# Kernel tuning notes

Measured on AMD Instinct MI355X. Metric: run time of the kernel, lower is better.

## Reference

```python
import jax, jax.numpy as jnp
import numpy as np

P = 1048576   # total sampled points
N = 8192      # rays
E = 8         # experts
H = 128       # expert hidden dim
TOP_K = 2
INTERVAL = 0.5      # stepsize * voxel_size_ratio
ACT_SHIFT = -4.0    # models[-1].act_shift
THRESH = 1e-4       # fast_color_thres (ndc=False)


def raw2alpha(d):
    # Raw2Alpha: alpha = 1 - exp(-softplus(density + act_shift) * interval)
    return 1.0 - jnp.exp(-jax.nn.softplus(d + ACT_SHIFT) * INTERVAL)


def alphas2weights(alpha, ray_id, n_rays):
    # Sequential per-ray transmittance: w_j = alpha_j * prod_{k<j in ray}(1 - alpha_k)
    la = jnp.log1p(-jnp.clip(alpha, 0.0, 1.0 - 1e-6))      # [P], <= 0
    cum = jnp.cumsum(la)
    excl = cum - la                                          # exclusive cumsum, nonincreasing
    # offset per ray = excl at first point of the (sorted) segment == segment max
    offset = jax.ops.segment_max(excl, ray_id, num_segments=n_rays)
    T = jnp.exp(excl - offset[ray_id])                       # transmittance before each point
    weights = alpha * T
    alphainv_last = jnp.exp(jax.ops.segment_sum(la, ray_id, num_segments=n_rays))
    return weights, alphainv_last


def setup_inputs() -> dict:
    key = jax.random.key(0)
    ks = jax.random.split(key, 12)
    s = 0.3  # weight scale keeping activations in a sane range
    return {
        "ray_pts": jax.random.uniform(ks[0], (P, 3), dtype=jnp.float32),
        "viewdirs": jax.random.normal(ks[1], (N, 3), dtype=jnp.float32),
        "bg": jnp.ones((3,), dtype=jnp.float32),
        "Wd1": jax.random.normal(ks[2], (3, H), dtype=jnp.float32) * s,
        "bd1": jnp.zeros((H,), dtype=jnp.float32),
        "Wd2": jax.random.normal(ks[3], (H, 1), dtype=jnp.float32) * s,
        "Wg": jax.random.normal(ks[4], (6, E), dtype=jnp.float32) * s,
        "We1": jax.random.normal(ks[5], (E, 6, H), dtype=jnp.float32) * s,
        "be1": jnp.zeros((E, H), dtype=jnp.float32),
        "Wrgb": jax.random.normal(ks[6], (E, H, 3), dtype=jnp.float32) * s,
        "Walpha": jax.random.normal(ks[7], (E, H, 1), dtype=jnp.float32) * s,
        "ray_id": jnp.sort(jax.random.randint(ks[8], (P,), 0, N)).astype(jnp.int32),
    }


def reference(ray_pts, viewdirs, bg, Wd1, bd1, Wd2, Wg, We1, be1, Wrgb, Walpha, ray_id):
    # --- density grid query + activation ---
    hd = jax.nn.relu(ray_pts @ Wd1 + bd1)                    # [P,H]
    density = (hd @ Wd2)[:, 0]                               # [P]
    alpha0 = raw2alpha(density)
    # filter low density (zeroing alpha == dropping the point from the cumprod)
    alpha0 = jnp.where(alpha0 > THRESH, alpha0, 0.0)
    w0, _ = alphas2weights(alpha0, ray_id, N)
    # filter low transmittance (w0 <= THRESH also covers alpha0 == 0)
    keep = w0 > THRESH                                        # [P] bool

    # --- gate: softmax over experts, top-k, renormalize ---
    x = jnp.concatenate([ray_pts, viewdirs[ray_id]], axis=-1)  # [P,6]
    probs = jax.nn.softmax(x @ Wg, axis=-1)                    # [P,E]
    vals, idx = jax.lax.top_k(probs, TOP_K)                    # [P,K]
    vals = vals / jnp.sum(vals, axis=-1, keepdims=True)        # top_k > 1
    g = jnp.sum(vals[..., None] * jax.nn.one_hot(idx, E, dtype=vals.dtype), axis=1)  # [P,E]
    g = g * keep[:, None].astype(g.dtype)

    # --- per-expert radiance / alpha, mixed by gate weights ---
    rgb = jnp.zeros((ray_pts.shape[0], 3), dtype=ray_pts.dtype)
    alpha_mix = jnp.zeros((ray_pts.shape[0],), dtype=ray_pts.dtype)
    for e in range(E):  # fixed small expert count
        h = jax.nn.relu(x @ We1[e] + be1[e])                   # [P,H]
        rgb_e = jax.nn.sigmoid(h @ Wrgb[e])                    # [P,3]
        a_e = raw2alpha((h @ Walpha[e])[:, 0])                 # [P]
        rgb = rgb + g[:, e:e + 1] * rgb_e
        alpha_mix = alpha_mix + g[:, e] * a_e

    # --- composite: Alphas2Weights + segment_coo sum + background ---
    w, alphainv_last = alphas2weights(alpha_mix, ray_id, N)
    rgb_marched = jax.ops.segment_sum(w[:, None] * rgb, ray_id, num_segments=N)
    rgb_marched = rgb_marched + alphainv_last[:, None] * bg
    return rgb_marched
```

## Files before the change

kernel.cpp:

```cpp
#include <hip/hip_runtime.h>

#define PTOT   1048576
#define NRAYS  8192
#define THRESH 1e-4f
#define ECAP   PTOT

typedef float F2 __attribute__((ext_vector_type(2)));

__device__ __forceinline__ F2 f2splat(float s){ F2 r; r.x = s; r.y = s; return r; }
__device__ __forceinline__ F2 f2fma(F2 a, float b, F2 c){
    return __builtin_elementwise_fma(a, f2splat(b), c);
}
__device__ __forceinline__ float raw2alpha_f(float d){
    return 1.0f - rsqrtf(1.0f + __expf(d - 4.0f));
}

__global__ __launch_bounds__(256) void k_point(
    const float* __restrict__ pts, const float* __restrict__ vdirs,
    const int* __restrict__ ray_id,
    const float* __restrict__ Wd1, const float* __restrict__ bd1,
    const float* __restrict__ Wd2, const float* __restrict__ Wg,
    float* __restrict__ alpha0, float* __restrict__ g0a, int* __restrict__ eea,
    int* __restrict__ ray_off)
{
    __shared__ float4 WD4[128];
    __shared__ float  WD2s[128];
    __shared__ float  WGs[8][6];
    int t = threadIdx.x;
    if (t < 128){
        WD4[t] = make_float4(Wd1[t], Wd1[128+t], Wd1[256+t], bd1[t]);
        WD2s[t] = Wd2[t];
    }
    if (t < 48) WGs[t & 7][t >> 3] = Wg[t];
    __syncthreads();

    int base = blockIdx.x * 1024 + t;
    F2 px[2], py[2], pz[2], vx[2], vy[2], vz[2], dens[2];
    int rid0[2], rid1[2];
    #pragma unroll
    for (int q=0;q<2;q++){
        int p0 = base + (2*q)*256, p1 = p0 + 256;
        px[q] = (F2){pts[3*p0],   pts[3*p1]};
        py[q] = (F2){pts[3*p0+1], pts[3*p1+1]};
        pz[q] = (F2){pts[3*p0+2], pts[3*p1+2]};
        int r0 = ray_id[p0], r1 = ray_id[p1];
        rid0[q] = r0; rid1[q] = r1;
        vx[q] = (F2){vdirs[3*r0],   vdirs[3*r1]};
        vy[q] = (F2){vdirs[3*r0+1], vdirs[3*r1+1]};
        vz[q] = (F2){vdirs[3*r0+2], vdirs[3*r1+2]};
        dens[q] = f2splat(0.f);
    }
    #pragma unroll
    for (int q=0;q<2;q++){
        int p0 = base + (2*q)*256, p1 = p0 + 256;
        int prev0 = (p0 == 0) ? -1 : ray_id[p0-1];
        if (prev0 != rid0[q]) for (int r=prev0+1; r<=rid0[q]; ++r) ray_off[r] = p0;
        int prev1 = ray_id[p1-1];
        if (prev1 != rid1[q]) for (int r=prev1+1; r<=rid1[q]; ++r) ray_off[r] = p1;
        if (p1 == PTOT-1) for (int r=rid1[q]+1; r<=NRAYS; ++r) ray_off[r] = PTOT;
    }
    #pragma unroll 2
    for (int i=0;i<128;i++){
        float4 w = WD4[i]; float w2 = WD2s[i];
        #pragma unroll
        for (int q=0;q<2;q++){
            F2 h = f2fma(px[q], w.x, f2fma(py[q], w.y, f2fma(pz[q], w.z, f2splat(w.w))));
            h = __builtin_elementwise_max(h, f2splat(0.f));
            dens[q] = f2fma(h, w2, dens[q]);
        }
    }
    #pragma unroll
    for (int q=0;q<2;q++){
        float a0 = raw2alpha_f(dens[q].x);
        float a1 = raw2alpha_f(dens[q].y);
        alpha0[base + (2*q)*256]   = (a0 > THRESH) ? a0 : 0.f;
        alpha0[base + (2*q+1)*256] = (a1 > THRESH) ? a1 : 0.f;
    }
    float m0[4], m1[4]; int i0[4], i1[4];
    #pragma unroll
    for (int j=0;j<4;j++){ m0[j]=-3.0e38f; m1[j]=-3.0e38f; i0[j]=0; i1[j]=0; }
    for (int e=0;e<8;e++){
        float w0=WGs[e][0],w1=WGs[e][1],w2=WGs[e][2],w3=WGs[e][3],w4=WGs[e][4],w5=WGs[e][5];
        #pragma unroll
        for (int q=0;q<2;q++){
            F2 l = f2fma(px[q],w0, f2fma(py[q],w1, f2fma(pz[q],w2,
                   f2fma(vx[q],w3, f2fma(vy[q],w4,
                   __builtin_elementwise_fma(vz[q], f2splat(w5), f2splat(0.f)))))));
            int j0 = 2*q, j1 = 2*q+1;
            float lx = l.x, ly = l.y;
            if (lx > m0[j0]){ m1[j0]=m0[j0]; i1[j0]=i0[j0]; m0[j0]=lx; i0[j0]=e; }
            else if (lx > m1[j0]){ m1[j0]=lx; i1[j0]=e; }
            if (ly > m0[j1]){ m1[j1]=m0[j1]; i1[j1]=i0[j1]; m0[j1]=ly; i0[j1]=e; }
            else if (ly > m1[j1]){ m1[j1]=ly; i1[j1]=e; }
        }
    }
    #pragma unroll
    for (int j=0;j<4;j++){
        float g0 = __fdividef(1.0f, 1.0f + __expf(m1[j]-m0[j]));
        g0a[base + j*256] = g0;
        eea[base + j*256] = i0[j] | (i1[j] << 8);
    }
}

__global__ __launch_bounds__(256) void k_scanfill(
    const float* __restrict__ alpha0, const int* __restrict__ eea,
    const float* __restrict__ g0a, const int* __restrict__ ray_off,
    unsigned char* __restrict__ keep, int* __restrict__ cntA,
    int2* __restrict__ ent)
{
    __shared__ int wcs[4][8];
    __shared__ int wb[4][8];
    int t = threadIdx.x, lane = t & 63, w = t >> 6;
    unsigned long long lt = (1ull << lane) - 1ull;
    int wid = blockIdx.x*4 + w;
    int s = ray_off[wid], e = ray_off[wid+1];

    int c[8];
    #pragma unroll
    for (int x=0;x<8;x++) c[x]=0;
    float carry = 1.f;
    for (int ch = s; ch < e; ch += 64){
        int p = ch + lane;
        bool in = p < e;
        float a = in ? alpha0[p] : 0.f;
        int  ee = in ? eea[p] : 0;
        float incl = 1.f - a;
        #pragma unroll
        for (int d=1; d<64; d<<=1){ float tt = __shfl_up(incl, d); if (lane >= d) incl *= tt; }
        float excl = __shfl_up(incl, 1); if (lane == 0) excl = 1.f;
        float w0 = a * carry * excl;
        int k = (in && w0 > THRESH) ? 1 : 0;
        if (in) keep[p] = (unsigned char)k;
        int e0 = ee & 255, e1 = (ee >> 8) & 255;
        #pragma unroll
        for (int x=0;x<8;x++){
            unsigned long long m0 = __ballot(k && e0==x);
            unsigned long long m1 = __ballot(k && e1==x);
            c[x] += __popcll(m0) + __popcll(m1);
        }
        carry *= __shfl(incl, 63);
    }
    if (lane == 0){
        #pragma unroll
        for (int x=0;x<8;x++) wcs[w][x] = c[x];
    }
    __syncthreads();
    if (t < 8){
        int tot = wcs[0][t]+wcs[1][t]+wcs[2][t]+wcs[3][t];
        int b = tot ? atomicAdd(&cntA[t], tot) : 0;
        wb[0][t] = b; b += wcs[0][t];
        wb[1][t] = b; b += wcs[1][t];
        wb[2][t] = b; b += wcs[2][t];
        wb[3][t] = b;
    }
    __syncthreads();
    int cur[8];
    #pragma unroll
    for (int x=0;x<8;x++) cur[x] = x*ECAP + wb[w][x];

    for (int ch = s; ch < e; ch += 64){
        int p = ch + lane;
        bool in = p < e;
        int  k  = in ? keep[p] : 0;
        int  ee = in ? eea[p] : 0;
        float g0 = in ? g0a[p] : 0.f;
        int e0 = ee & 255, e1 = (ee >> 8) & 255;
        #pragma unroll
        for (int x=0;x<8;x++){
            unsigned long long m0 = __ballot(k && e0==x);
            unsigned long long m1 = __ballot(k && e1==x);
            if (k && e0==x)
                ent[cur[x] + __popcll(m0 & lt)] = make_int2(p, __float_as_int(g0));
            if (k && e1==x)
                ent[cur[x] + __popcll(m0) + __popcll(m1 & lt)] =
                    make_int2(p | (1 << 30), __float_as_int(1.0f - g0));
            cur[x] += __popcll(m0) + __popcll(m1);
        }
    }
}

__global__ __launch_bounds__(256) void k_expert(
    const int2* __restrict__ ent, const int* __restrict__ cntA,
    const float* __restrict__ pts, const int* __restrict__ ray_id,
    const float* __restrict__ vdirs,
    const float* __restrict__ We1, const float* __restrict__ be1,
    const float* __restrict__ Wrgb, const float* __restrict__ Walpha,
    float4* __restrict__ res)
{
    int k = blockIdx.x;
    int e = -1, n = 0, base = 0;
    int acc = 0;
    #pragma unroll
    for (int i=0;i<8;i++){
        int c  = cntA[i];
        int ch = (c + 2047) >> 11;
        if (e < 0 && k < acc + ch){ e = i; n = c; base = (k - acc) << 11; }
        acc += ch;
    }
    if (e < 0) return;

    __shared__ float4 WA[128];
    __shared__ float4 WB[128];
    __shared__ float4 WC[128];
    int t = threadIdx.x;
    if (t < 128){
        const float* w = We1 + e*768;
        WA[t] = make_float4(w[t], w[128+t], w[256+t], w[384+t]);
        WB[t] = make_float4(w[512+t], w[640+t], be1[e*128+t], Walpha[e*128+t]);
        const float* wr = Wrgb + e*384 + 3*t;
        WC[t] = make_float4(wr[0], wr[1], wr[2], 0.f);
    }
    __syncthreads();
    const int2* eb = ent + (size_t)e * ECAP;

    F2 x0[4],x1[4],x2[4],x3[4],x4[4],x5[4];
    F2 ar[4],ag[4],ab[4],aa[4];
    #pragma unroll
    for (int pr=0;pr<4;pr++){
        int idx0 = base + t + (2*pr)*256, idx1 = idx0 + 256;
        int2 r0 = (idx0 < n) ? eb[idx0] : make_int2(0,0);
        int2 r1 = (idx1 < n) ? eb[idx1] : make_int2(0,0);
        int p0 = r0.x & 0x0FFFFFFF, p1 = r1.x & 0x0FFFFFFF;
        int ra = ray_id[p0], rb = ray_id[p1];
        x0[pr] = (F2){pts[3*p0],   pts[3*p1]};
        x1[pr] = (F2){pts[3*p0+1], pts[3*p1+1]};
        x2[pr] = (F2){pts[3*p0+2], pts[3*p1+2]};
        x3[pr] = (F2){vdirs[3*ra],   vdirs[3*rb]};
        x4[pr] = (F2){vdirs[3*ra+1], vdirs[3*rb+1]};
        x5[pr] = (F2){vdirs[3*ra+2], vdirs[3*rb+2]};
        ar[pr] = f2splat(0.f); ag[pr] = f2splat(0.f);
        ab[pr] = f2splat(0.f); aa[pr] = f2splat(0.f);
    }
    #pragma unroll 2
    for (int i=0;i<128;i++){
        float4 wa = WA[i], wb = WB[i], wc = WC[i];
        #pragma unroll
        for (int pr=0;pr<4;pr++){
            F2 h = f2fma(x0[pr],wa.x, f2fma(x1[pr],wa.y, f2fma(x2[pr],wa.z,
                   f2fma(x3[pr],wa.w, f2fma(x4[pr],wb.x, f2fma(x5[pr],wb.y,
                   f2splat(wb.z)))))));
            h = __builtin_elementwise_max(h, f2splat(0.f));
            ar[pr] = f2fma(h, wc.x, ar[pr]);
            ag[pr] = f2fma(h, wc.y, ag[pr]);
            ab[pr] = f2fma(h, wc.z, ab[pr]);
            aa[pr] = f2fma(h, wb.w, aa[pr]);
        }
    }
    #pragma unroll
    for (int pr=0;pr<4;pr++){
        #pragma unroll
        for (int sel=0; sel<2; sel++){
            int idx = base + t + (2*pr+sel)*256;
            if (idx < n){
                int2 rec = eb[idx];
                float vr = sel ? ar[pr].y : ar[pr].x;
                float vg = sel ? ag[pr].y : ag[pr].x;
                float vb = sel ? ab[pr].y : ab[pr].x;
                float va = sel ? aa[pr].y : aa[pr].x;
                float sr = __fdividef(1.0f, 1.0f + __expf(-vr));
                float sg = __fdividef(1.0f, 1.0f + __expf(-vg));
                float sb = __fdividef(1.0f, 1.0f + __expf(-vb));
                float a  = raw2alpha_f(va);
                float g  = __int_as_float(rec.y);
                int pp   = rec.x & 0x0FFFFFFF;
                int slot = ((unsigned)rec.x) >> 30;
                res[2*(size_t)pp + slot] = make_float4(g*sr, g*sg, g*sb, g*a);
            }
        }
    }
}

__global__ __launch_bounds__(256) void k_scan1(const float4* __restrict__ res,
                                               const unsigned char* __restrict__ keep,
                                               const int* __restrict__ ray_off,
                                               const float* __restrict__ bg,
                                               float* __restrict__ out)
{
    int wid  = (blockIdx.x*blockDim.x + threadIdx.x) >> 6;
    int lane = threadIdx.x & 63;
    if (wid >= NRAYS) return;
    int s = ray_off[wid], e = ray_off[wid+1];
    float carry = 1.f;
    float accx = 0.f, accy = 0.f, accz = 0.f;
    for (int c = s; c < e; c += 64){
        int p = c + lane;
        float4 v = make_float4(0.f,0.f,0.f,0.f);
        if (p < e && keep[p]){
            float4 v0 = res[2*(size_t)p];
            float4 v1 = res[2*(size_t)p + 1];
            v = make_float4(v0.x+v1.x, v0.y+v1.y, v0.z+v1.z, v0.w+v1.w);
        }
        float a = v.w;
        float incl = 1.f - a;
        #pragma unroll
        for (int d=1; d<64; d<<=1){ float tt = __shfl_up(incl, d); if (lane >= d) incl *= tt; }
        float excl = __shfl_up(incl, 1); if (lane == 0) excl = 1.f;
        float w = a * carry * excl;
        accx = fmaf(w, v.x, accx);
        accy = fmaf(w, v.y, accy);
        accz = fmaf(w, v.z, accz);
        carry *= __shfl(incl, 63);
    }
    #pragma unroll
    for (int d=32; d; d>>=1){
        accx += __shfl_xor(accx, d);
        accy += __shfl_xor(accy, d);
        accz += __shfl_xor(accz, d);
    }
    if (lane == 0){
        out[3*wid+0] = accx + carry*bg[0];
        out[3*wid+1] = accy + carry*bg[1];
        out[3*wid+2] = accz + carry*bg[2];
    }
}

extern "C" void kernel_launch(void* const* d_in, const int* in_sizes, int n_in,
                              void* d_out, int out_size, void* d_ws, size_t ws_size,
                              hipStream_t stream)
{
    const float* pts    = (const float*)d_in[0];
    const float* vdirs  = (const float*)d_in[1];
    const float* bg     = (const float*)d_in[2];
    const float* Wd1    = (const float*)d_in[3];
    const float* bd1    = (const float*)d_in[4];
    const float* Wd2    = (const float*)d_in[5];
    const float* Wg     = (const float*)d_in[6];
    const float* We1    = (const float*)d_in[7];
    const float* be1    = (const float*)d_in[8];
    const float* Wrgb   = (const float*)d_in[9];
    const float* Walpha = (const float*)d_in[10];
    const int*   ray_id = (const int*)d_in[11];
    float* out = (float*)d_out;

    char* ws = (char*)d_ws;
    size_t off = 0;
    unsigned char* keep  = (unsigned char*)(ws + off); off += (size_t)PTOT;
    int*   ray_off       = (int*)  (ws + off); off += 33024;
    int*   cntA          = (int*)  (ws + off); off += 256;
    off = (off + 255) & ~(size_t)255;
    size_t offA = off;
    float* alpha0        = (float*)(ws + offA);
    float* g0a           = (float*)(ws + offA + (size_t)PTOT*4);
    int*   eea           = (int*)  (ws + offA + (size_t)PTOT*8);
    float4* res          = (float4*)(ws + offA);
    size_t resBytes      = ((size_t)2*PTOT + 2) * 16;
    size_t offE          = (offA + resBytes + 255) & ~(size_t)255;
    int2*  ent           = (int2*) (ws + offE);

    hipMemsetAsync(cntA, 0, 256, stream);

    k_point   <<<PTOT/1024, 256, 0, stream>>>(pts, vdirs, ray_id, Wd1, bd1, Wd2, Wg,
                                              alpha0, g0a, eea, ray_off);
    k_scanfill<<<NRAYS/4, 256, 0, stream>>>(alpha0, eea, g0a, ray_off, keep, cntA, ent);
    k_expert  <<<1032, 256, 0, stream>>>(ent, cntA, pts, ray_id, vdirs,
                                         We1, be1, Wrgb, Walpha, res);
    k_scan1   <<<NRAYS*64/256, 256, 0, stream>>>(res, keep, ray_off, bg, out);
}
```

Before: 223.2 us.

## Fuse per-point density/gating into per-ray scan-fill kernel, split ray offsets out

```diff
diff --git a/kernel.cpp b/kernel.cpp
--- a/kernel.cpp
+++ b/kernel.cpp
@@ -4,6 +4,7 @@
 #define NRAYS  8192
 #define THRESH 1e-4f
 #define ECAP   PTOT
+#define WPTS   512
 
 typedef float F2 __attribute__((ext_vector_type(2)));
 
@@ -15,166 +16,169 @@
     return 1.0f - rsqrtf(1.0f + __expf(d - 4.0f));
 }
 
-__global__ __launch_bounds__(256) void k_point(
+__global__ __launch_bounds__(256) void k_rayoff(const int* __restrict__ ray_id,
+                                                int* __restrict__ ray_off)
+{
+    int p = blockIdx.x*256 + threadIdx.x;
+    int r = ray_id[p];
+    int prev = (p == 0) ? -1 : ray_id[p-1];
+    if (r != prev) for (int rr = prev+1; rr <= r; ++rr) ray_off[rr] = p;
+    if (p == PTOT-1) for (int rr = r+1; rr <= NRAYS; ++rr) ray_off[rr] = PTOT;
+}
+
+__global__ __launch_bounds__(256) void k_pointscan(
     const float* __restrict__ pts, const float* __restrict__ vdirs,
-    const int* __restrict__ ray_id,
     const float* __restrict__ Wd1, const float* __restrict__ bd1,
     const float* __restrict__ Wd2, const float* __restrict__ Wg,
-    float* __restrict__ alpha0, float* __restrict__ g0a, int* __restrict__ eea,
-    int* __restrict__ ray_off)
+    const int* __restrict__ ray_off,
+    unsigned char* __restrict__ keep, int* __restrict__ cntA,
+    int2* __restrict__ ent)
 {
     __shared__ float4 WD4[128];
     __shared__ float  WD2s[128];
     __shared__ float  WGs[8][6];
-    int t = threadIdx.x;
+    __shared__ int wcs[4][8];
+    __shared__ int wb[4][8];
+    __shared__ int sMaxW;
+    int t = threadIdx.x, lane = t & 63, w = t >> 6;
+    unsigned long long lt = (1ull << lane) - 1ull;
     if (t < 128){
         WD4[t] = make_float4(Wd1[t], Wd1[128+t], Wd1[256+t], bd1[t]);
         WD2s[t] = Wd2[t];
     }
     if (t < 48) WGs[t & 7][t >> 3] = Wg[t];
+    if (t == 0) sMaxW = 0;
     __syncthreads();
 
-    int base = blockIdx.x * 1024 + t;
-    F2 px[2], py[2], pz[2], vx[2], vy[2], vz[2], dens[2];
-    int rid0[2], rid1[2];
-    #pragma unroll
-    for (int q=0;q<2;q++){
-        int p0 = base + (2*q)*256, p1 = p0 + 256;
-        px[q] = (F2){pts[3*p0],   pts[3*p1]};
-        py[q] = (F2){pts[3*p0+1], pts[3*p1+1]};
-        pz[q] = (F2){pts[3*p0+2], pts[3*p1+2]};
-        int r0 = ray_id[p0], r1 = ray_id[p1];
-        rid0[q] = r0; rid1[q] = r1;
-        vx[q] = (F2){vdirs[3*r0],   vdirs[3*r1]};
-        vy[q] = (F2){vdirs[3*r0+1], vdirs[3*r1+1]};
-        vz[q] = (F2){vdirs[3*r0+2], vdirs[3*r1+2]};
-        dens[q] = f2splat(0.f);
-    }
-    #pragma unroll
-    for (int q=0;q<2;q++){
-        int p0 = base + (2*q)*256, p1 = p0 + 256;
-        int prev0 = (p0 == 0) ? -1 : ray_id[p0-1];
-        if (prev0 != rid0[q]) for (int r=prev0+1; r<=rid0[q]; ++r) ray_off[r] = p0;
-        int prev1 = ray_id[p1-1];
-        if (prev1 != rid1[q]) for (int r=prev1+1; r<=rid1[q]; ++r) ray_off[r] = p1;
-        if (p1 == PTOT-1) for (int r=rid1[q]+1; r<=NRAYS; ++r) ray_off[r] = PTOT;
-    }
-    #pragma unroll 2
-    for (int i=0;i<128;i++){
-        float4 w = WD4[i]; float w2 = WD2s[i];
-        #pragma unroll
-        for (int q=0;q<2;q++){
-            F2 h = f2fma(px[q], w.x, f2fma(py[q], w.y, f2fma(pz[q], w.z, f2splat(w.w))));
-            h = __builtin_elementwise_max(h, f2splat(0.f));
-            dens[q] = f2fma(h, w2, dens[q]);
-        }
-    }
-    #pragma unroll
-    for (int q=0;q<2;q++){
-        float a0 = raw2alpha_f(dens[q].x);
-        float a1 = raw2alpha_f(dens[q].y);
-        alpha0[base + (2*q)*256]   = (a0 > THRESH) ? a0 : 0.f;
-        alpha0[base + (2*q+1)*256] = (a1 > THRESH) ? a1 : 0.f;
-    }
-    float m0[4], m1[4]; int i0[4], i1[4];
-    #pragma unroll
-    for (int j=0;j<4;j++){ m0[j]=-3.0e38f; m1[j]=-3.0e38f; i0[j]=0; i1[j]=0; }
-    for (int e=0;e<8;e++){
-        float w0=WGs[e][0],w1=WGs[e][1],w2=WGs[e][2],w3=WGs[e][3],w4=WGs[e][4],w5=WGs[e][5];
-        #pragma unroll
-        for (int q=0;q<2;q++){
-            F2 l = f2fma(px[q],w0, f2fma(py[q],w1, f2fma(pz[q],w2,
-                   f2fma(vx[q],w3, f2fma(vy[q],w4,
-                   __builtin_elementwise_fma(vz[q], f2splat(w5), f2splat(0.f)))))));
-            int j0 = 2*q, j1 = 2*q+1;
-            float lx = l.x, ly = l.y;
-            if (lx > m0[j0]){ m1[j0]=m0[j0]; i1[j0]=i0[j0]; m0[j0]=lx; i0[j0]=e; }
-            else if (lx > m1[j0]){ m1[j0]=lx; i1[j0]=e; }
-            if (ly > m0[j1]){ m1[j1]=m0[j1]; i1[j1]=i0[j1]; m0[j1]=ly; i0[j1]=e; }
-            else if (ly > m1[j1]){ m1[j1]=ly; i1[j1]=e; }
-        }
-    }
-    #pragma unroll
-    for (int j=0;j<4;j++){
-        float g0 = __fdividef(1.0f, 1.0f + __expf(m1[j]-m0[j]));
-        g0a[base + j*256] = g0;
-        eea[base + j*256] = i0[j] | (i1[j] << 8);
-    }
-}
-
-__global__ __launch_bounds__(256) void k_scanfill(
-    const float* __restrict__ alpha0, const int* __restrict__ eea,
-    const float* __restrict__ g0a, const int* __restrict__ ray_off,
-    unsigned char* __restrict__ keep, int* __restrict__ cntA,
-    int2* __restrict__ ent)
-{
-    __shared__ int wcs[4][8];
-    __shared__ int wb[4][8];
-    int t = threadIdx.x, lane = t & 63, w = t >> 6;
-    unsigned long long lt = (1ull << lane) - 1ull;
     int wid = blockIdx.x*4 + w;
     int s = ray_off[wid], e = ray_off[wid+1];
-
-    int c[8];
-    #pragma unroll
-    for (int x=0;x<8;x++) c[x]=0;
+    float vx = vdirs[3*wid], vy = vdirs[3*wid+1], vz = vdirs[3*wid+2];
+    float goff[8];
+    #pragma unroll
+    for (int x=0;x<8;x++) goff[x] = vx*WGs[x][3] + vy*WGs[x][4] + vz*WGs[x][5];
+
+    int nw = (e > s) ? (e - s + WPTS - 1) / WPTS : 0;
+    if (lane == 0) atomicMax(&sMaxW, nw);
+    __syncthreads();
+    int wmax = sMaxW;
+
     float carry = 1.f;
-    for (int ch = s; ch < e; ch += 64){
-        int p = ch + lane;
-        bool in = p < e;
-        float a = in ? alpha0[p] : 0.f;
-        int  ee = in ? eea[p] : 0;
-        float incl = 1.f - a;
-        #pragma unroll
-        for (int d=1; d<64; d<<=1){ float tt = __shfl_up(incl, d); if (lane >= d) incl *= tt; }
-        float excl = __shfl_up(incl, 1); if (lane == 0) excl = 1.f;
-        float w0 = a * carry * excl;
-        int k = (in && w0 > THRESH) ? 1 : 0;
-        if (in) keep[p] = (unsigned char)k;
-        int e0 = ee & 255, e1 = (ee >> 8) & 255;
-        #pragma unroll
-        for (int x=0;x<8;x++){
-            unsigned long long m0 = __ballot(k && e0==x);
-            unsigned long long m1 = __ballot(k && e1==x);
-            c[x] += __popcll(m0) + __popcll(m1);
-        }
-        carry *= __shfl(incl, 63);
-    }
-    if (lane == 0){
-        #pragma unroll
-        for (int x=0;x<8;x++) wcs[w][x] = c[x];
-    }
-    __syncthreads();
-    if (t < 8){
-        int tot = wcs[0][t]+wcs[1][t]+wcs[2][t]+wcs[3][t];
-        int b = tot ? atomicAdd(&cntA[t], tot) : 0;
-        wb[0][t] = b; b += wcs[0][t];
-        wb[1][t] = b; b += wcs[1][t];
-        wb[2][t] = b; b += wcs[2][t];
-        wb[3][t] = b;
-    }
-    __syncthreads();
-    int cur[8];
-    #pragma unroll
-    for (int x=0;x<8;x++) cur[x] = x*ECAP + wb[w][x];
-
-    for (int ch = s; ch < e; ch += 64){
-        int p = ch + lane;
-        bool in = p < e;
-        int  k  = in ? keep[p] : 0;
-        int  ee = in ? eea[p] : 0;
-        float g0 = in ? g0a[p] : 0.f;
-        int e0 = ee & 255, e1 = (ee >> 8) & 255;
-        #pragma unroll
-        for (int x=0;x<8;x++){
-            unsigned long long m0 = __ballot(k && e0==x);
-            unsigned long long m1 = __ballot(k && e1==x);
-            if (k && e0==x)
-                ent[cur[x] + __popcll(m0 & lt)] = make_int2(p, __float_as_int(g0));
-            if (k && e1==x)
-                ent[cur[x] + __popcll(m0) + __popcll(m1 & lt)] =
-                    make_int2(p | (1 << 30), __float_as_int(1.0f - g0));
-            cur[x] += __popcll(m0) + __popcll(m1);
+    for (int win = 0; win < wmax; ++win){
+        int wbase = s + win*WPTS;
+        bool active = (wbase < e);
+
+        F2 av[4], gv[4]; int2 ev[4];
+        int kbits = 0;
+        int c[8];
+        #pragma unroll
+        for (int x=0;x<8;x++) c[x]=0;
+
+        #pragma unroll
+        for (int pp=0; pp<4; ++pp){
+            av[pp] = f2splat(0.f); gv[pp] = f2splat(0.f); ev[pp] = make_int2(0,0);
+            int pbase = wbase + pp*128;
+            if (active && pbase < e){
+                int p0 = pbase + lane, p1 = pbase + 64 + lane;
+                bool in0 = p0 < e, in1 = p1 < e;
+                F2 px = (F2){ in0 ? pts[3*p0]   : 0.f, in1 ? pts[3*p1]   : 0.f };
+                F2 py = (F2){ in0 ? pts[3*p0+1] : 0.f, in1 ? pts[3*p1+1] : 0.f };
+                F2 pz = (F2){ in0 ? pts[3*p0+2] : 0.f, in1 ? pts[3*p1+2] : 0.f };
+                F2 dens = f2splat(0.f);
+                #pragma unroll 2
+                for (int i=0;i<128;i++){
+                    float4 wv = WD4[i]; float w2 = WD2s[i];
+                    F2 h = f2fma(px, wv.x, f2fma(py, wv.y, f2fma(pz, wv.z, f2splat(wv.w))));
+                    h = __builtin_elementwise_max(h, f2splat(0.f));
+                    dens = f2fma(h, w2, dens);
+                }
+                float a0 = raw2alpha_f(dens.x); a0 = (a0 > THRESH) ? a0 : 0.f; if (!in0) a0 = 0.f;
+                float a1 = raw2alpha_f(dens.y); a1 = (a1 > THRESH) ? a1 : 0.f; if (!in1) a1 = 0.f;
+                av[pp] = (F2){a0, a1};
+                float m0a=-3.0e38f, m1a=-3.0e38f, m0b=-3.0e38f, m1b=-3.0e38f;
+                int i0a=0, i1a=0, i0b=0, i1b=0;
+                for (int x=0;x<8;x++){
+                    float w0=WGs[x][0], w1=WGs[x][1], w2g=WGs[x][2];
+                    F2 l = f2fma(px, w0, f2fma(py, w1,
+                           __builtin_elementwise_fma(pz, f2splat(w2g), f2splat(goff[x]))));
+                    float lx = l.x, ly = l.y;
+                    if (lx > m0a){ m1a=m0a; i1a=i0a; m0a=lx; i0a=x; }
+                    else if (lx > m1a){ m1a=lx; i1a=x; }
+                    if (ly > m0b){ m1b=m0b; i1b=i0b; m0b=ly; i0b=x; }
+                    else if (ly > m1b){ m1b=ly; i1b=x; }
+                }
+                float ga = __fdividef(1.0f, 1.0f + __expf(m1a-m0a));
+                float gb = __fdividef(1.0f, 1.0f + __expf(m1b-m0b));
+                gv[pp] = (F2){ga, gb};
+                ev[pp] = make_int2(i0a | (i1a << 8), i0b | (i1b << 8));
+            }
+        }
+
+        #pragma unroll
+        for (int pp=0; pp<4; ++pp){
+            #pragma unroll
+            for (int half=0; half<2; ++half){
+                int p = wbase + pp*128 + half*64 + lane;
+                bool in = active && (p < e);
+                float a = half ? av[pp].y : av[pp].x;
+                float incl = 1.f - a;
+                #pragma unroll
+                for (int d=1; d<64; d<<=1){ float tt = __shfl_up(incl, d); if (lane >= d) incl *= tt; }
+                float excl = __shfl_up(incl, 1); if (lane == 0) excl = 1.f;
+                float w0v = a * carry * excl;
+                int k = (in && w0v > THRESH) ? 1 : 0;
+                if (in) keep[p] = (unsigned char)k;
+                kbits |= k << (2*pp + half);
+                int eepk = half ? ev[pp].y : ev[pp].x;
+                int e0 = eepk & 255, e1 = (eepk >> 8) & 255;
+                #pragma unroll
+                for (int x=0;x<8;x++){
+                    unsigned long long m0 = __ballot(k && e0==x);
+                    unsigned long long m1 = __ballot(k && e1==x);
+                    c[x] += __popcll(m0) + __popcll(m1);
+                }
+                carry *= __shfl(incl, 63);
+            }
+        }
+
+        if (lane == 0){
+            #pragma unroll
+            for (int x=0;x<8;x++) wcs[w][x] = c[x];
+        }
+        __syncthreads();
+        if (t < 8){
+            int tot = wcs[0][t]+wcs[1][t]+wcs[2][t]+wcs[3][t];
+            int b = tot ? atomicAdd(&cntA[t], tot) : 0;
+            wb[0][t] = b; b += wcs[0][t];
+            wb[1][t] = b; b += wcs[1][t];
+            wb[2][t] = b; b += wcs[2][t];
+            wb[3][t] = b;
+        }
+        __syncthreads();
+        int cur[8];
+        #pragma unroll
+        for (int x=0;x<8;x++) cur[x] = x*ECAP + wb[w][x];
+
+        #pragma unroll
+        for (int pp=0; pp<4; ++pp){
+            #pragma unroll
+            for (int half=0; half<2; ++half){
+                int p = wbase + pp*128 + half*64 + lane;
+                int k = (kbits >> (2*pp + half)) & 1;
+                int eepk = half ? ev[pp].y : ev[pp].x;
+                float g0 = half ? gv[pp].y : gv[pp].x;
+                int e0 = eepk & 255, e1 = (eepk >> 8) & 255;
+                #pragma unroll
+                for (int x=0;x<8;x++){
+                    unsigned long long m0 = __ballot(k && e0==x);
+                    unsigned long long m1 = __ballot(k && e1==x);
+                    if (k && e0==x)
+                        ent[cur[x] + __popcll(m0 & lt)] = make_int2(p, __float_as_int(g0));
+                    if (k && e1==x)
+                        ent[cur[x] + __popcll(m0) + __popcll(m1 & lt)] =
+                            make_int2(p | (1 << 30), __float_as_int(1.0f - g0));
+                    cur[x] += __popcll(m0) + __popcll(m1);
+                }
+            }
         }
     }
 }
@@ -338,21 +342,16 @@
     int*   ray_off       = (int*)  (ws + off); off += 33024;
     int*   cntA          = (int*)  (ws + off); off += 256;
     off = (off + 255) & ~(size_t)255;
-    size_t offA = off;
-    float* alpha0        = (float*)(ws + offA);
-    float* g0a           = (float*)(ws + offA + (size_t)PTOT*4);
-    int*   eea           = (int*)  (ws + offA + (size_t)PTOT*8);
-    float4* res          = (float4*)(ws + offA);
-    size_t resBytes      = ((size_t)2*PTOT + 2) * 16;
-    size_t offE          = (offA + resBytes + 255) & ~(size_t)255;
-    int2*  ent           = (int2*) (ws + offE);
+    float4* res          = (float4*)(ws + off); off += ((size_t)2*PTOT + 2)*16;
+    off = (off + 255) & ~(size_t)255;
+    int2*  ent           = (int2*) (ws + off); off += (size_t)8*ECAP*8;
 
     hipMemsetAsync(cntA, 0, 256, stream);
 
-    k_point   <<<PTOT/1024, 256, 0, stream>>>(pts, vdirs, ray_id, Wd1, bd1, Wd2, Wg,
-                                              alpha0, g0a, eea, ray_off);
-    k_scanfill<<<NRAYS/4, 256, 0, stream>>>(alpha0, eea, g0a, ray_off, keep, cntA, ent);
-    k_expert  <<<1032, 256, 0, stream>>>(ent, cntA, pts, ray_id, vdirs,
-                                         We1, be1, Wrgb, Walpha, res);
-    k_scan1   <<<NRAYS*64/256, 256, 0, stream>>>(res, keep, ray_off, bg, out);
-}
+    k_rayoff   <<<PTOT/256, 256, 0, stream>>>(ray_id, ray_off);
+    k_pointscan<<<NRAYS/4, 256, 0, stream>>>(pts, vdirs, Wd1, bd1, Wd2, Wg,
+                                             ray_off, keep, cntA, ent);
+    k_expert   <<<1032, 256, 0, stream>>>(ent, cntA, pts, ray_id, vdirs,
+                                          We1, be1, Wrgb, Walpha, res);
+    k_scan1    <<<NRAYS*64/256, 256, 0, stream>>>(res, keep, ray_off, bg, out);
+}
```

Result: slower. 271.7 us (+21.7%).
